# Optimization experiments

Hardware: AMD Instinct MI355X
Metric: run time of the kernel (lower is better)

Reference implementation:

```python
import jax, jax.numpy as jnp
import numpy as np

SEQ = 8192
DIM = 1280
NHEADS = 16
HEAD_DIM = DIM // NHEADS  # 80
NSEG = 8
SEG = SEQ // NSEG  # 1024


def setup_inputs() -> dict:
    key = jax.random.key(0)
    ks = jax.random.split(key, 7)
    hidden_states = jax.random.normal(ks[0], (SEQ, DIM), jnp.float32)
    # realistic rotary embeddings: cos/sin of random angles, shape [S, head_dim]
    ang = jax.random.uniform(ks[1], (SEQ, HEAD_DIM), jnp.float32, 0.0, 2.0 * np.pi)
    cos = jnp.cos(ang)
    sin = jnp.sin(ang)
    qkv_w = jax.random.normal(ks[2], (3 * DIM, DIM), jnp.float32) * (DIM ** -0.5)
    qkv_b = jax.random.normal(ks[3], (3 * DIM,), jnp.float32) * 0.02
    proj_w = jax.random.normal(ks[4], (DIM, DIM), jnp.float32) * (DIM ** -0.5)
    proj_b = jax.random.normal(ks[5], (DIM,), jnp.float32) * 0.02
    cu_seqlens = jnp.arange(NSEG + 1, dtype=jnp.int32) * SEG  # equal segments
    return {"hidden_states": hidden_states, "cos": cos, "sin": sin,
            "qkv_w": qkv_w, "qkv_b": qkv_b, "proj_w": proj_w, "proj_b": proj_b,
            "cu_seqlens": cu_seqlens}


def _rope(x, cos, sin):
    # x: [S, H, D]; cos/sin: [S, D] broadcast over heads. Computed in fp32.
    x = x.astype(jnp.float32)
    d = x.shape[-1]
    x1, x2 = x[..., : d // 2], x[..., d // 2:]
    rot = jnp.concatenate([-x2, x1], axis=-1)
    return x * cos[:, None, :] + rot * sin[:, None, :]


def reference(hidden_states, cos, sin, qkv_w, qkv_b, proj_w, proj_b, cu_seqlens):
    S, dim = hidden_states.shape
    nseg = cu_seqlens.shape[0] - 1
    seg = S // nseg  # segments are equal-length; block-diagonal attention batches over them
    H, D = NHEADS, dim // NHEADS

    qkv = hidden_states @ qkv_w.T + qkv_b                 # [S, 3*dim]
    qkv = qkv.reshape(S, 3, H, D)
    q, k, v = qkv[:, 0], qkv[:, 1], qkv[:, 2]             # [S, H, D]

    in_dtype = hidden_states.dtype
    q = _rope(q, cos, sin).astype(in_dtype)
    k = _rope(k, cos, sin).astype(in_dtype)

    scale = D ** -0.5
    qs = q.reshape(nseg, seg, H, D)
    ks = k.reshape(nseg, seg, H, D)
    vs = v.reshape(nseg, seg, H, D)

    scores = jnp.einsum('bqhd,bkhd->bhqk', qs, ks) * scale  # [nseg, H, seg, seg]
    probs = jax.nn.softmax(scores, axis=-1)
    out = jnp.einsum('bhqk,bkhd->bqhd', probs, vs)          # [nseg, seg, H, D]
    out = out.reshape(S, H * D)
    return out @ proj_w.T + proj_b
```

## Files before the change

### kernel.cpp

```cpp
#include <hip/hip_runtime.h>

#define SEQ 8192
#define DIM 1280
#define NHEADS 16
#define HD 80
#define HDP 96
#define NSEG 8
#define SEG 1024
#define KVB 64
#define NSTEP (SEG / KVB)
#define PST 72

typedef float f32x4 __attribute__((ext_vector_type(4)));
typedef short bf16x8 __attribute__((ext_vector_type(8)));
typedef unsigned int u32;

__device__ __forceinline__ float fast_exp2(float x) {
  return __builtin_amdgcn_exp2f(x);
}

__device__ __forceinline__ short f2bf(float f) {
  unsigned int u = __builtin_bit_cast(unsigned int, f);
  u = (u + 0x7fff + ((u >> 16) & 1)) >> 16;
  return (short)u;
}

__device__ __forceinline__ float bf2f(short s) {
  u32 u = ((u32)(unsigned short)s) << 16;
  return __builtin_bit_cast(float, u);
}

__device__ __forceinline__ u32 cvt_pk_bf16(float lo, float hi) {
  u32 r;
  asm("v_cvt_pk_bf16_f32 %0, %1, %2" : "=v"(r) : "v"(lo), "v"(hi));
  return r;
}

typedef __attribute__((address_space(1))) const unsigned int glds_src_t;
typedef __attribute__((address_space(3))) unsigned int glds_dst_t;
__device__ __forceinline__ void gload_lds16(const void* g, void* l) {
  __builtin_amdgcn_global_load_lds((glds_src_t*)g, (glds_dst_t*)l, 16, 0, 0);
}

__global__ void cast_f32_bf16(const float* __restrict__ in, short* __restrict__ out, int n) {
  int n4 = n >> 2;
  for (int i = blockIdx.x * blockDim.x + threadIdx.x; i < n4; i += gridDim.x * blockDim.x) {
    float4 v = ((const float4*)in)[i];
    short4 o;
    o.x = f2bf(v.x); o.y = f2bf(v.y); o.z = f2bf(v.z); o.w = f2bf(v.w);
    ((short4*)out)[i] = o;
  }
}

__global__ __launch_bounds__(256) void gemm_bt_bias(
    const short* __restrict__ A, const short* __restrict__ B,
    const float* __restrict__ bias, float* __restrict__ C,
    short* __restrict__ Cb, int M, int N, int K) {
  __shared__ short As[2][128 * 64];
  __shared__ short Bs[2][128 * 64];
  int tid = threadIdx.x;
  int w = tid >> 6, l = tid & 63;
  int lrow = l & 15, lg = l >> 4;
  int bid = blockIdx.x;
  int cpx = gridDim.x >> 3;
  int lid = (bid & 7) * cpx + (bid >> 3);
  int ntx = N >> 7;
  int m0 = (lid / ntx) * 128, n0 = (lid % ntx) * 128;
  int wm = w & 1, wn = w >> 1;

  f32x4 acc[4][4] = {};

  const char* Abase = (const char*)A + (size_t)m0 * K * 2;
  const char* Bbase = (const char*)B + (size_t)n0 * K * 2;

#define STAGE_G(BUF, K0)                                                       \
  {                                                                            \
    _Pragma("unroll") for (int j = 0; j < 4; j++) {                            \
      int c = j * 256 + tid;                                                   \
      int row = c >> 3;                                                        \
      int slc = (c & 7) ^ (row & 7);                                           \
      size_t goff = (size_t)row * K * 2 + (size_t)(K0) * 2 + slc * 16;         \
      int loff = (j * 256 + w * 64) * 16;                                      \
      gload_lds16(Abase + goff, (char*)&As[BUF][0] + loff);                    \
      gload_lds16(Bbase + goff, (char*)&Bs[BUF][0] + loff);                    \
    }                                                                          \
  }

  STAGE_G(0, 0);
  __syncthreads();

  for (int k0 = 0; k0 < K; k0 += 64) {
    int cur = (k0 >> 6) & 1;
    if (k0 + 64 < K) {
      STAGE_G(cur ^ 1, k0 + 64);
    }
#pragma unroll
    for (int kk = 0; kk < 2; kk++) {
      bf16x8 a[4], b[4];
#pragma unroll
      for (int mt = 0; mt < 4; mt++) {
        int row = wm * 64 + mt * 16 + lrow;
        int p = (kk * 4 + lg) ^ (row & 7);
        a[mt] = *(const bf16x8*)&As[cur][row * 64 + p * 8];
      }
#pragma unroll
      for (int nt = 0; nt < 4; nt++) {
        int row = wn * 64 + nt * 16 + lrow;
        int p = (kk * 4 + lg) ^ (row & 7);
        b[nt] = *(const bf16x8*)&Bs[cur][row * 64 + p * 8];
      }
#pragma unroll
      for (int mt = 0; mt < 4; mt++)
#pragma unroll
        for (int nt = 0; nt < 4; nt++)
          acc[mt][nt] = __builtin_amdgcn_mfma_f32_16x16x32_bf16(a[mt], b[nt], acc[mt][nt], 0, 0, 0);
    }
    __syncthreads();
  }

#pragma unroll
  for (int nt = 0; nt < 4; nt++) {
    int col = n0 + wn * 64 + nt * 16 + lrow;
    float bv = bias[col];
#pragma unroll
    for (int mt = 0; mt < 4; mt++) {
      int mrow = m0 + wm * 64 + mt * 16 + lg * 4;
      if (Cb) {
#pragma unroll
        for (int r = 0; r < 4; r++)
          Cb[(size_t)(mrow + r) * N + col] = f2bf(acc[mt][nt][r] + bv);
      } else {
#pragma unroll
        for (int r = 0; r < 4; r++)
          C[(size_t)(mrow + r) * N + col] = acc[mt][nt][r] + bv;
      }
    }
  }
}

__global__ void rope_qk(const short* __restrict__ qkv, const float* __restrict__ cosb,
                        const float* __restrict__ sinb, short* __restrict__ qg,
                        short* __restrict__ kg) {
  int t = blockIdx.x * blockDim.x + threadIdx.x;
  if (t >= SEQ * NHEADS * 40) return;
  int d = t % 40;
  int h = (t / 40) & 15;
  int s = t / 640;
  const short* row = qkv + (size_t)s * (3 * DIM);
  float c0 = cosb[s * HD + d], c1 = cosb[s * HD + d + 40];
  float s0 = sinb[s * HD + d], s1 = sinb[s * HD + d + 40];
  float x1 = bf2f(row[h * HD + d]), x2 = bf2f(row[h * HD + d + 40]);
  float q0 = x1 * c0 - x2 * s0;
  float q1 = x2 * c1 + x1 * s1;
  float y1 = bf2f(row[DIM + h * HD + d]), y2 = bf2f(row[DIM + h * HD + d + 40]);
  float k0 = y1 * c0 - y2 * s0;
  float k1 = y2 * c1 + y1 * s1;
  const float sc = 0.11180339887498949f * 1.4426950408889634f;
  size_t base = ((size_t)h * SEQ + s) * HDP;
  qg[base + d] = f2bf(q0 * sc);
  qg[base + d + 40] = f2bf(q1 * sc);
  kg[base + d] = f2bf(k0);
  kg[base + d + 40] = f2bf(k1);
  if (d < 16) { qg[base + 80 + d] = 0; kg[base + 80 + d] = 0; }
}

__global__ void v_transpose(const short* __restrict__ qkv, short* __restrict__ vt) {
  __shared__ short T[16][72];
  int st = blockIdx.x, dt = blockIdx.y, h = blockIdx.z;
  int d0 = dt * 16, s0 = st * 64;
  int t = threadIdx.x;
  int dd = t & 15, ss = t >> 4;
#pragma unroll
  for (int j = 0; j < 4; j++) {
    int s = ss + j * 16;
    T[dd][s] = qkv[(size_t)(s0 + s) * (3 * DIM) + 2 * DIM + h * HD + d0 + dd];
  }
  __syncthreads();
  int s2 = t & 63, dr = t >> 6;
#pragma unroll
  for (int j = 0; j < 4; j++) {
    int d = dr + j * 4;
    vt[((size_t)(h * HD + d0 + d)) * SEQ + s0 + s2] = T[d][s2];
  }
}

__global__ __launch_bounds__(512, 2) void attn_kernel(
    const short* __restrict__ qg, const short* __restrict__ kg,
    const short* __restrict__ vt, short* __restrict__ out) {
  __shared__ short Ks[2][64 * 128];
  __shared__ short Pl[8][32 * PST];
  int bid = blockIdx.x;
  int b = bid & 7, h = (bid >> 3) & 15, qt = bid >> 7;
  int tid = threadIdx.x;
  int w = tid >> 6, l = tid & 63;
  int lrow = l & 15, lg = l >> 4;
  int qbase_s = b * SEG + qt * 256 + w * 32;

  const short* qh = qg + (size_t)h * SEQ * HDP;
  const short* kh = kg + (size_t)h * SEQ * HDP;
  const short* vh = vt + (size_t)h * HD * SEQ;

#define STAGE_K(BUF, KEY0N)                                                    \
  {                                                                            \
    _Pragma("unroll") for (int sr = 0; sr < 2; sr++) {                         \
      int sbase = sr * 512 + w * 64;                                           \
      int ss = sbase + l;                                                      \
      int skey = ss >> 4, sc = ss & 15;                                        \
      int slc = sc ^ (skey & 7);                                               \
      const short* ssrc =                                                      \
          kh + (size_t)((KEY0N) + skey) * HDP + (slc < 12 ? slc * 8 : 0);      \
      gload_lds16(ssrc, (char*)&Ks[BUF][0] + sbase * 16);                      \
    }                                                                          \
  }

  bf16x8 qf[2][3];
#pragma unroll
  for (int mt = 0; mt < 2; mt++)
#pragma unroll
    for (int ks = 0; ks < 3; ks++)
      qf[mt][ks] = *(const bf16x8*)&qh[(size_t)(qbase_s + mt * 16 + lrow) * HDP + ks * 32 + lg * 8];

  f32x4 o[2][5] = {};
  float m_st[2] = {-1e30f, -1e30f};
  float l_st[2] = {0.f, 0.f};

  short* Pw = &Pl[w][0];

  STAGE_K(0, b * SEG);
  __syncthreads();

  for (int i = 0; i < NSTEP; i++) {
    int cur = i & 1;
    int key0 = b * SEG + i * KVB;
    if (i + 1 < NSTEP) {
      STAGE_K(cur ^ 1, key0 + KVB);
    }

    f32x4 sv[2][4] = {};
    __builtin_amdgcn_s_setprio(1);
#pragma unroll
    for (int kt = 0; kt < 4; kt++) {
      bf16x8 kf[3];
      int key = kt * 16 + lrow;
#pragma unroll
      for (int ks = 0; ks < 3; ks++) {
        int p = (ks * 4 + lg) ^ (key & 7);
        kf[ks] = *(const bf16x8*)&Ks[cur][key * 128 + p * 8];
      }
#pragma unroll
      for (int mt = 0; mt < 2; mt++)
#pragma unroll
        for (int ks = 0; ks < 3; ks++)
          sv[mt][kt] = __builtin_amdgcn_mfma_f32_16x16x32_bf16(kf[ks], qf[mt][ks], sv[mt][kt], 0, 0, 0);
    }
    __builtin_amdgcn_s_setprio(0);

    bf16x8 vf[5][2];
#pragma unroll
    for (int nt = 0; nt < 5; nt++)
#pragma unroll
      for (int ks = 0; ks < 2; ks++)
        vf[nt][ks] = *(const bf16x8*)&vh[(size_t)(nt * 16 + lrow) * SEQ + key0 + ks * 32 + lg * 8];

    float cm[2];
#pragma unroll
    for (int mt = 0; mt < 2; mt++) {
      float a0 = fmaxf(fmaxf(sv[mt][0][0], sv[mt][0][1]), fmaxf(sv[mt][0][2], sv[mt][0][3]));
      float a1 = fmaxf(fmaxf(sv[mt][1][0], sv[mt][1][1]), fmaxf(sv[mt][1][2], sv[mt][1][3]));
      float a2 = fmaxf(fmaxf(sv[mt][2][0], sv[mt][2][1]), fmaxf(sv[mt][2][2], sv[mt][2][3]));
      float a3 = fmaxf(fmaxf(sv[mt][3][0], sv[mt][3][1]), fmaxf(sv[mt][3][2], sv[mt][3][3]));
      float c = fmaxf(fmaxf(a0, a1), fmaxf(a2, a3));
      c = fmaxf(c, __shfl_xor(c, 16));
      c = fmaxf(c, __shfl_xor(c, 32));
      cm[mt] = c;
    }
    if (__any((cm[0] > m_st[0] + 8.f) || (cm[1] > m_st[1] + 8.f))) {
#pragma unroll
      for (int mt = 0; mt < 2; mt++) {
        float mn = fmaxf(m_st[mt], cm[mt]);
        float c = fast_exp2(m_st[mt] - mn);
        m_st[mt] = mn;
        l_st[mt] *= c;
        float cr[4];
#pragma unroll
        for (int r = 0; r < 4; r++) cr[r] = __shfl(c, lg * 4 + r);
#pragma unroll
        for (int nt = 0; nt < 5; nt++)
#pragma unroll
          for (int r = 0; r < 4; r++) o[mt][nt][r] *= cr[r];
      }
    }
#pragma unroll
    for (int mt = 0; mt < 2; mt++) {
      float rs = 0.f;
#pragma unroll
      for (int kt = 0; kt < 4; kt++) {
#pragma unroll
        for (int r = 0; r < 4; r++) {
          sv[mt][kt][r] = fast_exp2(sv[mt][kt][r] - m_st[mt]);
          rs += sv[mt][kt][r];
        }
        uint2 pk;
        pk.x = cvt_pk_bf16(sv[mt][kt][0], sv[mt][kt][1]);
        pk.y = cvt_pk_bf16(sv[mt][kt][2], sv[mt][kt][3]);
        *(uint2*)&Pw[(mt * 16 + lrow) * PST + kt * 16 + lg * 4] = pk;
      }
      rs += __shfl_xor(rs, 16);
      rs += __shfl_xor(rs, 32);
      l_st[mt] += rs;
    }

    bf16x8 pa[2][2];
#pragma unroll
    for (int mt = 0; mt < 2; mt++)
#pragma unroll
      for (int ks = 0; ks < 2; ks++)
        pa[mt][ks] = *(const bf16x8*)&Pw[(mt * 16 + lrow) * PST + ks * 32 + lg * 8];
    __builtin_amdgcn_s_setprio(1);
#pragma unroll
    for (int nt = 0; nt < 5; nt++)
#pragma unroll
      for (int mt = 0; mt < 2; mt++)
#pragma unroll
        for (int ks = 0; ks < 2; ks++)
          o[mt][nt] = __builtin_amdgcn_mfma_f32_16x16x32_bf16(pa[mt][ks], vf[nt][ks], o[mt][nt], 0, 0, 0);
    __builtin_amdgcn_s_setprio(0);

    __syncthreads();
  }

#pragma unroll
  for (int mt = 0; mt < 2; mt++) {
    float rl = 1.f / l_st[mt];
    float ir[4];
#pragma unroll
    for (int r = 0; r < 4; r++) ir[r] = __shfl(rl, lg * 4 + r);
#pragma unroll
    for (int r = 0; r < 4; r++) {
      int srow = qbase_s + mt * 16 + lg * 4 + r;
#pragma unroll
      for (int nt = 0; nt < 5; nt++)
        out[(size_t)srow * DIM + h * HD + nt * 16 + lrow] = f2bf(o[mt][nt][r] * ir[r]);
    }
  }
}

extern "C" void kernel_launch(void* const* d_in, const int* in_sizes, int n_in,
                              void* d_out, int out_size, void* d_ws, size_t ws_size,
                              hipStream_t stream) {
  const float* hidden = (const float*)d_in[0];
  const float* cosb = (const float*)d_in[1];
  const float* sinb = (const float*)d_in[2];
  const float* qkv_w = (const float*)d_in[3];
  const float* qkv_b = (const float*)d_in[4];
  const float* proj_w = (const float*)d_in[5];
  const float* proj_b = (const float*)d_in[6];

  char* ws = (char*)d_ws;
  short* qkv_bf = (short*)(ws);
  short* attn_o = (short*)(ws);
  short* wp_bf = (short*)(ws + 23068672);
  short* q_bf = (short*)(ws + 125829120);
  short* k_bf = (short*)(ws + 150994944);
  short* v_tb = (short*)(ws + 176160768);
  short* h_bf = (short*)(ws + 197132288);
  short* wq_bf = (short*)(ws + 218103808);

  cast_f32_bf16<<<4096, 256, 0, stream>>>(hidden, h_bf, SEQ * DIM);
  cast_f32_bf16<<<4096, 256, 0, stream>>>(qkv_w, wq_bf, 3 * DIM * DIM);
  gemm_bt_bias<<<1920, 256, 0, stream>>>(h_bf, wq_bf, qkv_b, nullptr, qkv_bf, SEQ, 3 * DIM, DIM);
  rope_qk<<<20480, 256, 0, stream>>>(qkv_bf, cosb, sinb, q_bf, k_bf);
  v_transpose<<<dim3(128, 5, 16), 256, 0, stream>>>(qkv_bf, v_tb);
  cast_f32_bf16<<<2048, 256, 0, stream>>>(proj_w, wp_bf, DIM * DIM);
  attn_kernel<<<512, 512, 0, stream>>>(q_bf, k_bf, v_tb, attn_o);
  gemm_bt_bias<<<640, 256, 0, stream>>>(attn_o, wp_bf, proj_b, (float*)d_out, nullptr, SEQ, DIM, DIM);
}
```

Baseline: 321.7 us.

## Restructure GEMM to 256x128 tiles with 8 waves and LDS-staged bf16 epilogue

```diff
diff --git a/kernel.cpp b/kernel.cpp
--- a/kernel.cpp
+++ b/kernel.cpp
@@ -52,84 +52,106 @@
   }
 }
 
-__global__ __launch_bounds__(256) void gemm_bt_bias(
+__global__ __launch_bounds__(512, 2) void gemm_bt_bias(
     const short* __restrict__ A, const short* __restrict__ B,
     const float* __restrict__ bias, float* __restrict__ C,
     short* __restrict__ Cb, int M, int N, int K) {
-  __shared__ short As[2][128 * 64];
-  __shared__ short Bs[2][128 * 64];
+  __shared__ short Sh[24576];
   int tid = threadIdx.x;
   int w = tid >> 6, l = tid & 63;
   int lrow = l & 15, lg = l >> 4;
+  int wm = w >> 2, wn = w & 3;
   int bid = blockIdx.x;
   int cpx = gridDim.x >> 3;
   int lid = (bid & 7) * cpx + (bid >> 3);
   int ntx = N >> 7;
-  int m0 = (lid / ntx) * 128, n0 = (lid % ntx) * 128;
-  int wm = w & 1, wn = w >> 1;
-
-  f32x4 acc[4][4] = {};
+  int m0 = (lid / ntx) * 256, n0 = (lid % ntx) * 128;
+
+  f32x4 acc[8][2] = {};
 
   const char* Abase = (const char*)A + (size_t)m0 * K * 2;
   const char* Bbase = (const char*)B + (size_t)n0 * K * 2;
 
-#define STAGE_G(BUF, K0)                                                       \
-  {                                                                            \
-    _Pragma("unroll") for (int j = 0; j < 4; j++) {                            \
-      int c = j * 256 + tid;                                                   \
-      int row = c >> 3;                                                        \
-      int slc = (c & 7) ^ (row & 7);                                           \
-      size_t goff = (size_t)row * K * 2 + (size_t)(K0) * 2 + slc * 16;         \
-      int loff = (j * 256 + w * 64) * 16;                                      \
-      gload_lds16(Abase + goff, (char*)&As[BUF][0] + loff);                    \
-      gload_lds16(Bbase + goff, (char*)&Bs[BUF][0] + loff);                    \
-    }                                                                          \
-  }
-
-  STAGE_G(0, 0);
-  __syncthreads();
-
   for (int k0 = 0; k0 < K; k0 += 64) {
-    int cur = (k0 >> 6) & 1;
-    if (k0 + 64 < K) {
-      STAGE_G(cur ^ 1, k0 + 64);
-    }
+#pragma unroll
+    for (int j = 0; j < 4; j++) {
+      int c = j * 512 + tid;
+      int row = c >> 3;
+      int slc = (c & 7) ^ (row & 7);
+      gload_lds16(Abase + (size_t)row * K * 2 + (size_t)k0 * 2 + slc * 16,
+                  (char*)Sh + (j * 512 + w * 64) * 16);
+    }
+#pragma unroll
+    for (int j = 0; j < 2; j++) {
+      int c = j * 512 + tid;
+      int row = c >> 3;
+      int slc = (c & 7) ^ (row & 7);
+      gload_lds16(Bbase + (size_t)row * K * 2 + (size_t)k0 * 2 + slc * 16,
+                  (char*)Sh + 32768 + (j * 512 + w * 64) * 16);
+    }
+    asm volatile("s_waitcnt vmcnt(0)" ::: "memory");
+    __builtin_amdgcn_s_barrier();
+    asm volatile("" ::: "memory");
 #pragma unroll
     for (int kk = 0; kk < 2; kk++) {
-      bf16x8 a[4], b[4];
-#pragma unroll
-      for (int mt = 0; mt < 4; mt++) {
-        int row = wm * 64 + mt * 16 + lrow;
+      bf16x8 a[8], b[2];
+#pragma unroll
+      for (int mt = 0; mt < 8; mt++) {
+        int row = wm * 128 + mt * 16 + lrow;
         int p = (kk * 4 + lg) ^ (row & 7);
-        a[mt] = *(const bf16x8*)&As[cur][row * 64 + p * 8];
-      }
-#pragma unroll
-      for (int nt = 0; nt < 4; nt++) {
-        int row = wn * 64 + nt * 16 + lrow;
+        a[mt] = *(const bf16x8*)&Sh[row * 64 + p * 8];
+      }
+#pragma unroll
+      for (int nt = 0; nt < 2; nt++) {
+        int row = wn * 32 + nt * 16 + lrow;
         int p = (kk * 4 + lg) ^ (row & 7);
-        b[nt] = *(const bf16x8*)&Bs[cur][row * 64 + p * 8];
-      }
-#pragma unroll
-      for (int mt = 0; mt < 4; mt++)
-#pragma unroll
-        for (int nt = 0; nt < 4; nt++)
+        b[nt] = *(const bf16x8*)&Sh[16384 + row * 64 + p * 8];
+      }
+      __builtin_amdgcn_s_setprio(1);
+#pragma unroll
+      for (int mt = 0; mt < 8; mt++)
+#pragma unroll
+        for (int nt = 0; nt < 2; nt++)
           acc[mt][nt] = __builtin_amdgcn_mfma_f32_16x16x32_bf16(a[mt], b[nt], acc[mt][nt], 0, 0, 0);
-    }
-    __syncthreads();
-  }
-
-#pragma unroll
-  for (int nt = 0; nt < 4; nt++) {
-    int col = n0 + wn * 64 + nt * 16 + lrow;
-    float bv = bias[col];
-#pragma unroll
-    for (int mt = 0; mt < 4; mt++) {
-      int mrow = m0 + wm * 64 + mt * 16 + lg * 4;
-      if (Cb) {
-#pragma unroll
-        for (int r = 0; r < 4; r++)
-          Cb[(size_t)(mrow + r) * N + col] = f2bf(acc[mt][nt][r] + bv);
-      } else {
+      __builtin_amdgcn_s_setprio(0);
+    }
+    __builtin_amdgcn_s_barrier();
+    asm volatile("" ::: "memory");
+  }
+
+  if (Cb) {
+#pragma unroll
+    for (int half = 0; half < 2; half++) {
+      __syncthreads();
+      if (wm == half) {
+#pragma unroll
+        for (int mt = 0; mt < 8; mt++)
+#pragma unroll
+          for (int nt = 0; nt < 2; nt++) {
+            int col = wn * 32 + nt * 16 + lrow;
+            float bv = bias[n0 + col];
+#pragma unroll
+            for (int r = 0; r < 4; r++)
+              Sh[(mt * 16 + lg * 4 + r) * 136 + col] = f2bf(acc[mt][nt][r] + bv);
+          }
+      }
+      __syncthreads();
+#pragma unroll
+      for (int j = 0; j < 4; j++) {
+        int c = j * 512 + tid;
+        int row = c >> 4, ch = c & 15;
+        *(uint4*)&Cb[(size_t)(m0 + half * 128 + row) * N + n0 + ch * 8] =
+            *(const uint4*)&Sh[row * 136 + ch * 8];
+      }
+    }
+  } else {
+#pragma unroll
+    for (int nt = 0; nt < 2; nt++) {
+      int col = n0 + wn * 32 + nt * 16 + lrow;
+      float bv = bias[col];
+#pragma unroll
+      for (int mt = 0; mt < 8; mt++) {
+        int mrow = m0 + wm * 128 + mt * 16 + lg * 4;
 #pragma unroll
         for (int r = 0; r < 4; r++)
           C[(size_t)(mrow + r) * N + col] = acc[mt][nt][r] + bv;
@@ -368,10 +390,10 @@
 
   cast_f32_bf16<<<4096, 256, 0, stream>>>(hidden, h_bf, SEQ * DIM);
   cast_f32_bf16<<<4096, 256, 0, stream>>>(qkv_w, wq_bf, 3 * DIM * DIM);
-  gemm_bt_bias<<<1920, 256, 0, stream>>>(h_bf, wq_bf, qkv_b, nullptr, qkv_bf, SEQ, 3 * DIM, DIM);
+  gemm_bt_bias<<<960, 512, 0, stream>>>(h_bf, wq_bf, qkv_b, nullptr, qkv_bf, SEQ, 3 * DIM, DIM);
   rope_qk<<<20480, 256, 0, stream>>>(qkv_bf, cosb, sinb, q_bf, k_bf);
   v_transpose<<<dim3(128, 5, 16), 256, 0, stream>>>(qkv_bf, v_tb);
   cast_f32_bf16<<<2048, 256, 0, stream>>>(proj_w, wp_bf, DIM * DIM);
   attn_kernel<<<512, 512, 0, stream>>>(q_bf, k_bf, v_tb, attn_o);
-  gemm_bt_bias<<<640, 256, 0, stream>>>(attn_o, wp_bf, proj_b, (float*)d_out, nullptr, SEQ, DIM, DIM);
-}
+  gemm_bt_bias<<<320, 512, 0, stream>>>(attn_o, wp_bf, proj_b, (float*)d_out, nullptr, SEQ, DIM, DIM);
+}
```

Measured after the change: 376.5 us. 1.17x slower.
